# Optimization experiments

Measured on AMD Instinct MI355X. Metric: run time of the kernel, lower is better.

Reference implementation:

```python
import jax, jax.numpy as jnp
import numpy as np

N = 8192
D = 256
DENSITY = 0.02  # ~164 neighbors per node


def setup_inputs() -> dict:
    key = jax.random.key(0)
    k1, k2, k3, k4 = jax.random.split(key, 4)
    inputs = jax.random.normal(k1, (N, D), dtype=jnp.float32)
    vals = jax.random.uniform(k2, (N, N), dtype=jnp.float32, minval=0.1, maxval=1.0)
    mask = jax.random.uniform(k3, (N, N), dtype=jnp.float32) < DENSITY
    adj = jnp.where(mask, vals, 0.0)
    H_v = 0.1 * jax.random.normal(k4, (D, 1), dtype=jnp.float32)
    return {"inputs": inputs, "adj": adj, "H_v": H_v}


def reference(inputs, adj, H_v):
    # scores[j] = inputs[j] . H_v  -> sparse values v_ij = adj_ij * scores[j]
    scores = jnp.squeeze(inputs @ H_v, -1)            # [N]
    mask = adj != 0.0                                  # nonzero pattern of SparseTensor
    logits = adj * scores[None, :]                     # [N, N]
    neg = jnp.asarray(jnp.finfo(logits.dtype).min, logits.dtype)
    logits = jnp.where(mask, logits, neg)
    # sparse softmax: normalize only over nonzero entries per row
    m = jnp.max(logits, axis=1, keepdims=True)
    e = jnp.where(mask, jnp.exp(logits - m), 0.0)
    s = jnp.sum(e, axis=1, keepdims=True)
    weights = e / jnp.where(s > 0, s, 1.0)             # empty rows -> all-zero weights
    # sparse_tensor_dense_matmul(weights, inputs)
    return weights @ inputs                            # [N, D]
```

## Files before the change

### kernel.cpp

```cpp
#include <hip/hip_runtime.h>

#define NN 8192
#define DD 256
#define RCAP 512

typedef float v4f __attribute__((ext_vector_type(4)));
typedef unsigned short u16x4 __attribute__((ext_vector_type(4)));

__device__ __forceinline__ unsigned short f2bf_rne(float x) {
    unsigned u = __float_as_uint(x);
    u += 0x7fffu + ((u >> 16) & 1u);
    return (unsigned short)(u >> 16);
}

__device__ __forceinline__ float4 bf4_to_f4(u16x4 u) {
    float4 r;
    r.x = __uint_as_float((unsigned)u.x << 16);
    r.y = __uint_as_float((unsigned)u.y << 16);
    r.z = __uint_as_float((unsigned)u.z << 16);
    r.w = __uint_as_float((unsigned)u.w << 16);
    return r;
}

template <bool WRITE_IB>
__global__ __launch_bounds__(256) void prep_kernel(const float* __restrict__ inputs,
                                                   const float* __restrict__ Hv,
                                                   float* __restrict__ scores,
                                                   unsigned short* __restrict__ ib) {
    int wave = threadIdx.x >> 6;
    int lane = threadIdx.x & 63;
    int row  = blockIdx.x * 4 + wave;
    float4 v = ((const float4*)(inputs + (size_t)row * DD))[lane];
    if (WRITE_IB) {
        u16x4 u;
        u.x = f2bf_rne(v.x); u.y = f2bf_rne(v.y); u.z = f2bf_rne(v.z); u.w = f2bf_rne(v.w);
        ((u16x4*)(ib + (size_t)row * DD))[lane] = u;
    }
    float4 h = ((const float4*)Hv)[lane];
    float s = v.x * h.x + v.y * h.y + v.z * h.z + v.w * h.w;
    #pragma unroll
    for (int off = 32; off > 0; off >>= 1) s += __shfl_down(s, off, 64);
    if (lane == 0) scores[row] = s;
}

__global__ __launch_bounds__(256) void build_kernel(const float* __restrict__ adj,
                                                    const float* __restrict__ scores,
                                                    float2* __restrict__ csr,
                                                    int* __restrict__ cnt) {
    __shared__ float2 s_ja[RCAP];
    __shared__ int s_wsum[4];

    const int row  = blockIdx.x;
    const int tid  = threadIdx.x;
    const int lane = tid & 63;
    const int wave = tid >> 6;

    const v4f* arow4 = (const v4f*)(adj + (size_t)row * NN);
    v4f a[8];
#pragma unroll
    for (int c = 0; c < 8; ++c) a[c] = arow4[c * 256 + tid];

    int nz = 0;
#pragma unroll
    for (int c = 0; c < 8; ++c)
        nz += (a[c].x != 0.f) + (a[c].y != 0.f) + (a[c].z != 0.f) + (a[c].w != 0.f);

    int pre = nz;
#pragma unroll
    for (int off = 1; off < 64; off <<= 1) {
        int t = __shfl_up(pre, off, 64);
        if (lane >= off) pre += t;
    }
    if (lane == 63) s_wsum[wave] = pre;
    __syncthreads();
    int base = 0, total = 0;
#pragma unroll
    for (int w = 0; w < 4; ++w) {
        int t = s_wsum[w];
        if (w < wave) base += t;
        total += t;
    }

    int off = base + pre - nz;
#pragma unroll
    for (int c = 0; c < 8; ++c) {
        int j0 = c * 1024 + tid * 4;
        float v;
        v = a[c].x; if (v != 0.f) { if (off < RCAP) s_ja[off] = make_float2(__int_as_float(j0 + 0), v); off++; }
        v = a[c].y; if (v != 0.f) { if (off < RCAP) s_ja[off] = make_float2(__int_as_float(j0 + 1), v); off++; }
        v = a[c].z; if (v != 0.f) { if (off < RCAP) s_ja[off] = make_float2(__int_as_float(j0 + 2), v); off++; }
        v = a[c].w; if (v != 0.f) { if (off < RCAP) s_ja[off] = make_float2(__int_as_float(j0 + 3), v); off++; }
    }
    __syncthreads();

    int lim = total <= RCAP ? total : RCAP;
    for (int k = tid; k < lim; k += 256) {
        float2 ja = s_ja[k];
        int j = __float_as_int(ja.x);
        float e = __expf(ja.y * scores[j]);
        csr[(size_t)row * RCAP + k] = make_float2(ja.x, e);
    }
    if (tid == 0) cnt[row] = total;
}

__device__ __forceinline__ void gather_range(const float2* __restrict__ entries,
                                             int kbeg, int kend,
                                             const unsigned short* __restrict__ ib,
                                             int lane, int lane4,
                                             float4& acc, float& ssum) {
    for (int b = kbeg; b < kend; b += 64) {
        int nb = kend - b; nb = nb > 64 ? 64 : nb;
        float2 je = entries[b + (lane < nb ? lane : 0)];
        int jl = __float_as_int(je.x);
        int el = __float_as_int(je.y);
        int m = 0;
        for (; m + 8 <= nb; m += 8) {
            int js[8]; float es[8]; float4 f[8];
            #pragma unroll
            for (int u = 0; u < 8; ++u) {
                js[u] = __builtin_amdgcn_readlane(jl, m + u);
                es[u] = __uint_as_float(__builtin_amdgcn_readlane(el, m + u));
            }
            #pragma unroll
            for (int u = 0; u < 8; ++u)
                f[u] = bf4_to_f4(*(const u16x4*)(ib + (size_t)js[u] * DD + lane4));
            #pragma unroll
            for (int u = 0; u < 8; ++u) {
                acc.x += es[u] * f[u].x; acc.y += es[u] * f[u].y;
                acc.z += es[u] * f[u].z; acc.w += es[u] * f[u].w;
                ssum  += es[u];
            }
        }
        for (; m < nb; ++m) {
            int   j = __builtin_amdgcn_readlane(jl, m);
            float e = __uint_as_float(__builtin_amdgcn_readlane(el, m));
            float4 f = bf4_to_f4(*(const u16x4*)(ib + (size_t)j * DD + lane4));
            acc.x += e * f.x; acc.y += e * f.y; acc.z += e * f.z; acc.w += e * f.w;
            ssum += e;
        }
    }
}

__global__ __launch_bounds__(256) void gather_kernel(const float2* __restrict__ csr,
                                                     const int* __restrict__ cnt,
                                                     const unsigned short* __restrict__ ib,
                                                     const float* __restrict__ adj,
                                                     const float* __restrict__ scores,
                                                     float* __restrict__ out) {
    __shared__ float  s_red[4 * DD];
    __shared__ float  s_ssum[4];
    __shared__ float2 s_je[1024];
    __shared__ int    s_cnt;

    const int row   = blockIdx.x;
    const int tid   = threadIdx.x;
    const int lane  = tid & 63;
    const int wave  = tid >> 6;
    const int lane4 = lane * 4;

    int total = cnt[row];
    float4 acc = make_float4(0.f, 0.f, 0.f, 0.f);
    float ssum = 0.f;

    if (total <= RCAP) {
        const float2* rowp = csr + (size_t)row * RCAP;
        gather_range(rowp, wave * total / 4, (wave + 1) * total / 4,
                     ib, lane, lane4, acc, ssum);
    } else {
        const float* arow = adj + (size_t)row * NN;
        for (int c = 0; c < 8; ++c) {
            if (tid == 0) s_cnt = 0;
            __syncthreads();
            float4 a = ((const float4*)(arow + c * 1024))[tid];
            int j0 = c * 1024 + tid * 4;
            float v;
            v = a.x; if (v != 0.f) { int k = atomicAdd(&s_cnt, 1); s_je[k] = make_float2(__int_as_float(j0 + 0), __expf(v * scores[j0 + 0])); }
            v = a.y; if (v != 0.f) { int k = atomicAdd(&s_cnt, 1); s_je[k] = make_float2(__int_as_float(j0 + 1), __expf(v * scores[j0 + 1])); }
            v = a.z; if (v != 0.f) { int k = atomicAdd(&s_cnt, 1); s_je[k] = make_float2(__int_as_float(j0 + 2), __expf(v * scores[j0 + 2])); }
            v = a.w; if (v != 0.f) { int k = atomicAdd(&s_cnt, 1); s_je[k] = make_float2(__int_as_float(j0 + 3), __expf(v * scores[j0 + 3])); }
            __syncthreads();
            int tc = s_cnt;
            gather_range(s_je, wave * tc / 4, (wave + 1) * tc / 4,
                         ib, lane, lane4, acc, ssum);
            __syncthreads();
        }
    }

    if (lane == 0) s_ssum[wave] = ssum;
    *(float4*)&s_red[wave * DD + lane4] = acc;
    __syncthreads();
    float tot = s_ssum[0] + s_ssum[1] + s_ssum[2] + s_ssum[3];
    float r = s_red[0 * DD + tid] + s_red[1 * DD + tid] + s_red[2 * DD + tid] + s_red[3 * DD + tid];
    out[(size_t)row * DD + tid] = (tot > 0.f) ? r / tot : 0.f;
}

__global__ __launch_bounds__(256) void attn_fallback(const float* __restrict__ adj,
                                                     const float* __restrict__ inputs,
                                                     const float* __restrict__ scores,
                                                     float* __restrict__ out) {
    __shared__ int   s_j[1024];
    __shared__ float s_e[1024];
    __shared__ int   s_cnt;
    const int row = blockIdx.x;
    const int tid = threadIdx.x;
    const float* arow = adj + (size_t)row * NN;
    float acc = 0.f, ssum = 0.f;
    for (int base = 0; base < NN; base += 1024) {
        if (tid == 0) s_cnt = 0;
        __syncthreads();
        float4 a = ((const float4*)(arow + base))[tid];
        int j0 = base + tid * 4;
        if (a.x != 0.f) { int k = atomicAdd(&s_cnt, 1); s_j[k] = j0 + 0; s_e[k] = __expf(a.x * scores[j0 + 0]); }
        if (a.y != 0.f) { int k = atomicAdd(&s_cnt, 1); s_j[k] = j0 + 1; s_e[k] = __expf(a.y * scores[j0 + 1]); }
        if (a.z != 0.f) { int k = atomicAdd(&s_cnt, 1); s_j[k] = j0 + 2; s_e[k] = __expf(a.z * scores[j0 + 2]); }
        if (a.w != 0.f) { int k = atomicAdd(&s_cnt, 1); s_j[k] = j0 + 3; s_e[k] = __expf(a.w * scores[j0 + 3]); }
        __syncthreads();
        int c = s_cnt;
        for (int k = 0; k < c; ++k) {
            float e = s_e[k];
            acc  += e * inputs[(size_t)s_j[k] * DD + tid];
            ssum += e;
        }
        __syncthreads();
    }
    out[(size_t)row * DD + tid] = (ssum > 0.f) ? acc / ssum : 0.f;
}

extern "C" void kernel_launch(void* const* d_in, const int* in_sizes, int n_in,
                              void* d_out, int out_size, void* d_ws, size_t ws_size,
                              hipStream_t stream) {
    const float* inputs = (const float*)d_in[0];
    const float* adj    = (const float*)d_in[1];
    const float* Hv     = (const float*)d_in[2];
    float* out = (float*)d_out;

    char* ws = (char*)d_ws;
    float*          scores = (float*)ws;
    unsigned short* ib     = (unsigned short*)(ws + 32768);
    int*            cnt    = (int*)(ws + 32768 + (size_t)NN * DD * 2);
    float2*         csr    = (float2*)(ws + 65536 + (size_t)NN * DD * 2);

    const size_t need = 65536 + (size_t)NN * DD * 2 + (size_t)NN * RCAP * sizeof(float2);

    if (ws_size >= need) {
        prep_kernel<true><<<NN / 4, 256, 0, stream>>>(inputs, Hv, scores, ib);
        build_kernel<<<NN, 256, 0, stream>>>(adj, scores, csr, cnt);
        gather_kernel<<<NN, 256, 0, stream>>>(csr, cnt, ib, adj, scores, out);
    } else {
        prep_kernel<false><<<NN / 4, 256, 0, stream>>>(inputs, Hv, scores, nullptr);
        attn_fallback<<<NN, 256, 0, stream>>>(adj, inputs, scores, out);
    }
}
```

Measured before the change: 410.1 us.

## Process two rows per block in build and gather kernels with interleaved gathers

The build kernel now handles two adjacency rows per block and issues both rows' loads up front using nontemporal loads. The gather kernel processes two rows per block and interleaves their 8-wide gather batches. The goal is more memory-level parallelism and latency hiding for the random bf16 row gathers, plus less streaming-cache pollution from the 256MB adjacency read. The cost is higher register pressure, an extra barrier per row, and half as many blocks.

```diff
diff --git a/kernel.cpp b/kernel.cpp
--- a/kernel.cpp
+++ b/kernel.cpp
@@ -43,23 +43,11 @@
     if (lane == 0) scores[row] = s;
 }
 
-__global__ __launch_bounds__(256) void build_kernel(const float* __restrict__ adj,
-                                                    const float* __restrict__ scores,
-                                                    float2* __restrict__ csr,
-                                                    int* __restrict__ cnt) {
-    __shared__ float2 s_ja[RCAP];
-    __shared__ int s_wsum[4];
-
-    const int row  = blockIdx.x;
-    const int tid  = threadIdx.x;
-    const int lane = tid & 63;
-    const int wave = tid >> 6;
-
-    const v4f* arow4 = (const v4f*)(adj + (size_t)row * NN);
-    v4f a[8];
-#pragma unroll
-    for (int c = 0; c < 8; ++c) a[c] = arow4[c * 256 + tid];
-
+
+__device__ __forceinline__ void process_row(const v4f a[8], int row, int tid, int lane, int wave,
+                                            const float* __restrict__ scores,
+                                            float2* __restrict__ csr, int* __restrict__ cnt,
+                                            float2* s_ja, int* s_wsum) {
     int nz = 0;
 #pragma unroll
     for (int c = 0; c < 8; ++c)
@@ -101,43 +89,108 @@
         csr[(size_t)row * RCAP + k] = make_float2(ja.x, e);
     }
     if (tid == 0) cnt[row] = total;
-}
-
-__device__ __forceinline__ void gather_range(const float2* __restrict__ entries,
-                                             int kbeg, int kend,
-                                             const unsigned short* __restrict__ ib,
-                                             int lane, int lane4,
-                                             float4& acc, float& ssum) {
-    for (int b = kbeg; b < kend; b += 64) {
-        int nb = kend - b; nb = nb > 64 ? 64 : nb;
-        float2 je = entries[b + (lane < nb ? lane : 0)];
-        int jl = __float_as_int(je.x);
-        int el = __float_as_int(je.y);
-        int m = 0;
-        for (; m + 8 <= nb; m += 8) {
-            int js[8]; float es[8]; float4 f[8];
-            #pragma unroll
-            for (int u = 0; u < 8; ++u) {
-                js[u] = __builtin_amdgcn_readlane(jl, m + u);
-                es[u] = __uint_as_float(__builtin_amdgcn_readlane(el, m + u));
-            }
-            #pragma unroll
-            for (int u = 0; u < 8; ++u)
-                f[u] = bf4_to_f4(*(const u16x4*)(ib + (size_t)js[u] * DD + lane4));
-            #pragma unroll
-            for (int u = 0; u < 8; ++u) {
-                acc.x += es[u] * f[u].x; acc.y += es[u] * f[u].y;
-                acc.z += es[u] * f[u].z; acc.w += es[u] * f[u].w;
-                ssum  += es[u];
-            }
-        }
-        for (; m < nb; ++m) {
-            int   j = __builtin_amdgcn_readlane(jl, m);
-            float e = __uint_as_float(__builtin_amdgcn_readlane(el, m));
-            float4 f = bf4_to_f4(*(const u16x4*)(ib + (size_t)j * DD + lane4));
-            acc.x += e * f.x; acc.y += e * f.y; acc.z += e * f.z; acc.w += e * f.w;
-            ssum += e;
-        }
+    __syncthreads();
+}
+
+__global__ __launch_bounds__(256) void build_kernel(const float* __restrict__ adj,
+                                                    const float* __restrict__ scores,
+                                                    float2* __restrict__ csr,
+                                                    int* __restrict__ cnt) {
+    __shared__ float2 s_ja[RCAP];
+    __shared__ int s_wsum[4];
+
+    const int tid  = threadIdx.x;
+    const int lane = tid & 63;
+    const int wave = tid >> 6;
+    const int row0 = blockIdx.x * 2;
+
+    const v4f* p0 = (const v4f*)(adj + (size_t)row0 * NN);
+    const v4f* p1 = (const v4f*)(adj + (size_t)(row0 + 1) * NN);
+    v4f a0[8], a1[8];
+#pragma unroll
+    for (int c = 0; c < 8; ++c) a0[c] = __builtin_nontemporal_load(&p0[c * 256 + tid]);
+#pragma unroll
+    for (int c = 0; c < 8; ++c) a1[c] = __builtin_nontemporal_load(&p1[c * 256 + tid]);
+
+    process_row(a0, row0,     tid, lane, wave, scores, csr, cnt, s_ja, s_wsum);
+    process_row(a1, row0 + 1, tid, lane, wave, scores, csr, cnt, s_ja, s_wsum);
+}
+
+
+__device__ __forceinline__ void batch8(const unsigned short* __restrict__ ib,
+                                       int jl, int el, int m, int lane4,
+                                       float4& acc, float& ssum) {
+    int js[8]; float es[8]; float4 f[8];
+#pragma unroll
+    for (int u = 0; u < 8; ++u) {
+        js[u] = __builtin_amdgcn_readlane(jl, m + u);
+        es[u] = __uint_as_float(__builtin_amdgcn_readlane(el, m + u));
+    }
+#pragma unroll
+    for (int u = 0; u < 8; ++u)
+        f[u] = bf4_to_f4(*(const u16x4*)(ib + (size_t)js[u] * DD + lane4));
+#pragma unroll
+    for (int u = 0; u < 8; ++u) {
+        acc.x += es[u] * f[u].x; acc.y += es[u] * f[u].y;
+        acc.z += es[u] * f[u].z; acc.w += es[u] * f[u].w;
+        ssum  += es[u];
+    }
+}
+
+__device__ void gather_pair(const float2* __restrict__ eA, int bA, int keA,
+                            const float2* __restrict__ eB, int bB, int keB,
+                            const unsigned short* __restrict__ ib,
+                            int lane, int lane4,
+                            float4& accA, float& ssA, float4& accB, float& ssB) {
+    while (bA < keA || bB < keB) {
+        int nA = keA - bA; nA = nA > 64 ? 64 : nA;
+        int nB = keB - bB; nB = nB > 64 ? 64 : nB;
+        int jlA = 0, elA = 0, jlB = 0, elB = 0;
+        if (nA > 0) {
+            float2 je = eA[bA + (lane < nA ? lane : 0)];
+            if (lane >= nA) je.y = 0.f;
+            jlA = __float_as_int(je.x); elA = __float_as_int(je.y);
+        }
+        if (nB > 0) {
+            float2 je = eB[bB + (lane < nB ? lane : 0)];
+            if (lane >= nB) je.y = 0.f;
+            jlB = __float_as_int(je.x); elB = __float_as_int(je.y);
+        }
+        int nA8 = nA > 0 ? ((nA + 7) & ~7) : 0;
+        int nB8 = nB > 0 ? ((nB + 7) & ~7) : 0;
+        int mx = nA8 > nB8 ? nA8 : nB8;
+        for (int m = 0; m < mx; m += 8) {
+            if (m < nA8) batch8(ib, jlA, elA, m, lane4, accA, ssA);
+            if (m < nB8) batch8(ib, jlB, elB, m, lane4, accB, ssB);
+        }
+        if (nA > 0) bA += nA;
+        if (nB > 0) bB += nB;
+    }
+}
+
+__device__ void slow_row(const float* __restrict__ adj, int row,
+                         const float* __restrict__ scores,
+                         const unsigned short* __restrict__ ib,
+                         float2* s_je, int* s_cnt,
+                         int tid, int lane, int lane4, int wave,
+                         float4& acc, float& ssum) {
+    const float* arow = adj + (size_t)row * NN;
+    for (int c = 0; c < 8; ++c) {
+        if (tid == 0) *s_cnt = 0;
+        __syncthreads();
+        float4 a = ((const float4*)(arow + c * 1024))[tid];
+        int j0 = c * 1024 + tid * 4;
+        float v;
+        v = a.x; if (v != 0.f) { int k = atomicAdd(s_cnt, 1); s_je[k] = make_float2(__int_as_float(j0 + 0), __expf(v * scores[j0 + 0])); }
+        v = a.y; if (v != 0.f) { int k = atomicAdd(s_cnt, 1); s_je[k] = make_float2(__int_as_float(j0 + 1), __expf(v * scores[j0 + 1])); }
+        v = a.z; if (v != 0.f) { int k = atomicAdd(s_cnt, 1); s_je[k] = make_float2(__int_as_float(j0 + 2), __expf(v * scores[j0 + 2])); }
+        v = a.w; if (v != 0.f) { int k = atomicAdd(s_cnt, 1); s_je[k] = make_float2(__int_as_float(j0 + 3), __expf(v * scores[j0 + 3])); }
+        __syncthreads();
+        int tc = *s_cnt;
+        float4 dummy = make_float4(0.f, 0.f, 0.f, 0.f); float sdummy = 0.f;
+        gather_pair(s_je, wave * tc / 4, (wave + 1) * tc / 4,
+                    s_je, 0, 0, ib, lane, lane4, acc, ssum, dummy, sdummy);
+        __syncthreads();
     }
 }
 
@@ -147,51 +200,54 @@
                                                      const float* __restrict__ adj,
                                                      const float* __restrict__ scores,
                                                      float* __restrict__ out) {
-    __shared__ float  s_red[4 * DD];
-    __shared__ float  s_ssum[4];
+    __shared__ float  s_red[2][4 * DD];
+    __shared__ float  s_ss[2][4];
     __shared__ float2 s_je[1024];
     __shared__ int    s_cnt;
 
-    const int row   = blockIdx.x;
     const int tid   = threadIdx.x;
     const int lane  = tid & 63;
     const int wave  = tid >> 6;
     const int lane4 = lane * 4;
-
-    int total = cnt[row];
-    float4 acc = make_float4(0.f, 0.f, 0.f, 0.f);
-    float ssum = 0.f;
-
-    if (total <= RCAP) {
-        const float2* rowp = csr + (size_t)row * RCAP;
-        gather_range(rowp, wave * total / 4, (wave + 1) * total / 4,
-                     ib, lane, lane4, acc, ssum);
+    const int row0  = blockIdx.x * 2;
+    const int row1  = row0 + 1;
+
+    int t0 = cnt[row0];
+    int t1 = cnt[row1];
+    float4 acc0 = make_float4(0.f, 0.f, 0.f, 0.f), acc1 = acc0;
+    float ss0 = 0.f, ss1 = 0.f;
+
+    if (t0 <= RCAP && t1 <= RCAP) {
+        gather_pair(csr + (size_t)row0 * RCAP, wave * t0 / 4, (wave + 1) * t0 / 4,
+                    csr + (size_t)row1 * RCAP, wave * t1 / 4, (wave + 1) * t1 / 4,
+                    ib, lane, lane4, acc0, ss0, acc1, ss1);
     } else {
-        const float* arow = adj + (size_t)row * NN;
-        for (int c = 0; c < 8; ++c) {
-            if (tid == 0) s_cnt = 0;
-            __syncthreads();
-            float4 a = ((const float4*)(arow + c * 1024))[tid];
-            int j0 = c * 1024 + tid * 4;
-            float v;
-            v = a.x; if (v != 0.f) { int k = atomicAdd(&s_cnt, 1); s_je[k] = make_float2(__int_as_float(j0 + 0), __expf(v * scores[j0 + 0])); }
-            v = a.y; if (v != 0.f) { int k = atomicAdd(&s_cnt, 1); s_je[k] = make_float2(__int_as_float(j0 + 1), __expf(v * scores[j0 + 1])); }
-            v = a.z; if (v != 0.f) { int k = atomicAdd(&s_cnt, 1); s_je[k] = make_float2(__int_as_float(j0 + 2), __expf(v * scores[j0 + 2])); }
-            v = a.w; if (v != 0.f) { int k = atomicAdd(&s_cnt, 1); s_je[k] = make_float2(__int_as_float(j0 + 3), __expf(v * scores[j0 + 3])); }
-            __syncthreads();
-            int tc = s_cnt;
-            gather_range(s_je, wave * tc / 4, (wave + 1) * tc / 4,
-                         ib, lane, lane4, acc, ssum);
-            __syncthreads();
-        }
-    }
-
-    if (lane == 0) s_ssum[wave] = ssum;
-    *(float4*)&s_red[wave * DD + lane4] = acc;
+        if (t0 <= RCAP) {
+            float4 d = make_float4(0.f, 0.f, 0.f, 0.f); float sd = 0.f;
+            gather_pair(csr + (size_t)row0 * RCAP, wave * t0 / 4, (wave + 1) * t0 / 4,
+                        csr, 0, 0, ib, lane, lane4, acc0, ss0, d, sd);
+        } else {
+            slow_row(adj, row0, scores, ib, s_je, &s_cnt, tid, lane, lane4, wave, acc0, ss0);
+        }
+        if (t1 <= RCAP) {
+            float4 d = make_float4(0.f, 0.f, 0.f, 0.f); float sd = 0.f;
+            gather_pair(csr + (size_t)row1 * RCAP, wave * t1 / 4, (wave + 1) * t1 / 4,
+                        csr, 0, 0, ib, lane, lane4, acc1, ss1, d, sd);
+        } else {
+            slow_row(adj, row1, scores, ib, s_je, &s_cnt, tid, lane, lane4, wave, acc1, ss1);
+        }
+    }
+
+    if (lane == 0) { s_ss[0][wave] = ss0; s_ss[1][wave] = ss1; }
+    *(float4*)&s_red[0][wave * DD + lane4] = acc0;
+    *(float4*)&s_red[1][wave * DD + lane4] = acc1;
     __syncthreads();
-    float tot = s_ssum[0] + s_ssum[1] + s_ssum[2] + s_ssum[3];
-    float r = s_red[0 * DD + tid] + s_red[1 * DD + tid] + s_red[2 * DD + tid] + s_red[3 * DD + tid];
-    out[(size_t)row * DD + tid] = (tot > 0.f) ? r / tot : 0.f;
+    float tot0 = s_ss[0][0] + s_ss[0][1] + s_ss[0][2] + s_ss[0][3];
+    float tot1 = s_ss[1][0] + s_ss[1][1] + s_ss[1][2] + s_ss[1][3];
+    float r0 = s_red[0][0 * DD + tid] + s_red[0][1 * DD + tid] + s_red[0][2 * DD + tid] + s_red[0][3 * DD + tid];
+    float r1 = s_red[1][0 * DD + tid] + s_red[1][1 * DD + tid] + s_red[1][2 * DD + tid] + s_red[1][3 * DD + tid];
+    out[(size_t)row0 * DD + tid] = (tot0 > 0.f) ? r0 / tot0 : 0.f;
+    out[(size_t)row1 * DD + tid] = (tot1 > 0.f) ? r1 / tot1 : 0.f;
 }
 
 __global__ __launch_bounds__(256) void attn_fallback(const float* __restrict__ adj,
@@ -244,8 +300,8 @@
 
     if (ws_size >= need) {
         prep_kernel<true><<<NN / 4, 256, 0, stream>>>(inputs, Hv, scores, ib);
-        build_kernel<<<NN, 256, 0, stream>>>(adj, scores, csr, cnt);
-        gather_kernel<<<NN, 256, 0, stream>>>(csr, cnt, ib, adj, scores, out);
+        build_kernel<<<NN / 2, 256, 0, stream>>>(adj, scores, csr, cnt);
+        gather_kernel<<<NN / 2, 256, 0, stream>>>(csr, cnt, ib, adj, scores, out);
     } else {
         prep_kernel<false><<<NN / 4, 256, 0, stream>>>(inputs, Hv, scores, nullptr);
         attn_fallback<<<NN, 256, 0, stream>>>(adj, inputs, scores, out);
```

Measured after the change: 397.4 us. 3.1% less time.
